# Kernel tuning notes

Hardware: AMD Instinct MI355X
Metric: run time of the kernel (lower is better)

## Reference

```python
import jax, jax.numpy as jnp
import numpy as np

N_NODES = 100000
N_EDGES = 640000
IN_FEATS = 128
OUT_FEATS = 128


def setup_inputs() -> dict:
    key = jax.random.key(0)
    k1, k2, k3 = jax.random.split(key, 3)
    feat = jax.random.normal(k1, (N_NODES, IN_FEATS), dtype=jnp.float32)
    edge_src = jax.random.randint(k2, (N_EDGES,), 0, N_NODES, dtype=jnp.int64)
    edge_dst = jax.random.randint(k3, (N_EDGES,), 0, N_NODES, dtype=jnp.int64)
    # init.constant_(weight, 1) / init.constant_(bias, 1) in the original module
    weight = jnp.ones((OUT_FEATS, IN_FEATS), dtype=jnp.float32)
    bias = jnp.ones((OUT_FEATS,), dtype=jnp.float32)
    return {"feat": feat, "edge_src": edge_src, "edge_dst": edge_dst,
            "weight": weight, "bias": bias}


def reference(feat, edge_src, edge_dst, weight, bias):
    # copy_u: message on each edge is the source node's feature  [E, F_in]
    msgs = feat[edge_src]
    # sum reduce messages into destination nodes                 [N_V, F_in]
    h = jax.ops.segment_sum(msgs, edge_dst, num_segments=N_NODES)
    # linear: h @ W^T + b                                        [N_V, F_out]
    return h @ weight.T + bias
```

## Files before the change

kernel.cpp:

```cpp
#include <hip/hip_runtime.h>

#define F 128
#define STRIDE 32

typedef __bf16 bf8 __attribute__((ext_vector_type(8)));
typedef __bf16 bf4 __attribute__((ext_vector_type(4)));
typedef float f4 __attribute__((ext_vector_type(4)));
typedef unsigned short us8 __attribute__((ext_vector_type(8)));

__global__ void zero_int(int* __restrict__ p, int n) {
  int i = blockIdx.x * blockDim.x + threadIdx.x;
  if (i < n) p[i] = 0;
}

__global__ void zero_f4(float4* __restrict__ p, int n4) {
  int i = blockIdx.x * blockDim.x + threadIdx.x;
  if (i < n4) p[i] = make_float4(0.f, 0.f, 0.f, 0.f);
}

__global__ __launch_bounds__(256, 4) void transform_build(
    const float* __restrict__ feat, const float* __restrict__ W,
    __bf16* __restrict__ tf, const int* __restrict__ esrc,
    const int* __restrict__ edst, int* __restrict__ cnt,
    int* __restrict__ bucket, int n_rows, int nN, int nE) {
  __shared__ bf8 wlds[2048];
  const int tid = threadIdx.x;
  const int lane = tid & 63;
  const int wid = tid >> 6;
  const int lr = lane & 15;
  const int hi = lane >> 4;
  const int lk = hi * 8;

  const int e0 = blockIdx.x * 512 + tid;
  const int e1 = e0 + 256;
  int d0 = -1, d1 = -1, s0 = 0, s1 = 0;
  if (e0 < nE) { d0 = edst[e0]; s0 = esrc[e0]; }
  if (e1 < nE) { d1 = edst[e1]; s1 = esrc[e1]; }

  const int r0 = blockIdx.x * 64 + wid * 16;
  int arow = r0 + lr;
  if (arow >= n_rows) arow = n_rows - 1;
  if (arow < 0) arow = 0;
  const float* hr = feat + (size_t)arow * F;
  float4 u[8];
#pragma unroll
  for (int kk = 0; kk < 4; ++kk) {
    u[kk * 2]     = *(const float4*)(hr + kk * 32 + lk);
    u[kk * 2 + 1] = *(const float4*)(hr + kk * 32 + lk + 4);
  }

  int p0 = (d0 >= 0) ? atomicAdd(&cnt[d0], 1) : STRIDE;
  int p1 = (d1 >= 0) ? atomicAdd(&cnt[d1], 1) : STRIDE;

#pragma unroll
  for (int i = 0; i < 8; ++i) {
    int fid = tid + i * 256;
    int fl = fid & 63;
    int kkt = fid >> 6;
    int kk = kkt & 3;
    int t = kkt >> 2;
    const float* wr = W + (size_t)(t * 16 + (fl & 15)) * F + kk * 32 + (fl >> 4) * 8;
    float4 w0 = *(const float4*)wr;
    float4 w1 = *(const float4*)(wr + 4);
    bf8 b;
    b[0] = (__bf16)w0.x; b[1] = (__bf16)w0.y;
    b[2] = (__bf16)w0.z; b[3] = (__bf16)w0.w;
    b[4] = (__bf16)w1.x; b[5] = (__bf16)w1.y;
    b[6] = (__bf16)w1.z; b[7] = (__bf16)w1.w;
    wlds[fid] = b;
  }
  __syncthreads();

  if (p0 < STRIDE) bucket[(size_t)p0 * nN + d0] = s0;
  if (p1 < STRIDE) bucket[(size_t)p1 * nN + d1] = s1;

  if (r0 >= n_rows) return;

  bf8 af[4];
#pragma unroll
  for (int kk = 0; kk < 4; ++kk) {
    bf8 a;
    a[0] = (__bf16)u[kk * 2].x;     a[1] = (__bf16)u[kk * 2].y;
    a[2] = (__bf16)u[kk * 2].z;     a[3] = (__bf16)u[kk * 2].w;
    a[4] = (__bf16)u[kk * 2 + 1].x; a[5] = (__bf16)u[kk * 2 + 1].y;
    a[6] = (__bf16)u[kk * 2 + 1].z; a[7] = (__bf16)u[kk * 2 + 1].w;
    af[kk] = a;
  }

  f4 acc[8];
#pragma unroll
  for (int t = 0; t < 8; ++t) acc[t] = (f4){0.f, 0.f, 0.f, 0.f};
#pragma unroll
  for (int kk = 0; kk < 4; ++kk)
#pragma unroll
    for (int t = 0; t < 8; ++t)
      acc[t] = __builtin_amdgcn_mfma_f32_16x16x32_bf16(
          wlds[(t * 4 + kk) * 64 + lane], af[kk], acc[t], 0, 0, 0);

  const int r = r0 + lr;
  if (r < n_rows) {
    __bf16* dst = tf + (size_t)r * F + hi * 4;
#pragma unroll
    for (int t = 0; t < 8; ++t) {
      bf4 p;
      p[0] = (__bf16)acc[t][0];
      p[1] = (__bf16)acc[t][1];
      p[2] = (__bf16)acc[t][2];
      p[3] = (__bf16)acc[t][3];
      *(bf4*)(dst + t * 16) = p;
    }
  }
}

__device__ inline void addrow(float* a, us8 v) {
#pragma unroll
  for (int j = 0; j < 8; ++j) a[j] += __uint_as_float((unsigned)v[j] << 16);
}

__global__ __launch_bounds__(256) void aggregate_bf16(
    const __bf16* __restrict__ tf, const int* __restrict__ cnt,
    const int* __restrict__ bucket, const float* __restrict__ bias,
    float* __restrict__ out, int nN) {
  long long gid = (long long)blockIdx.x * 256 + threadIdx.x;
  int node = (int)(gid >> 4);
  int c = (int)(gid & 15);
  if (node >= nN) return;
  int n = cnt[node];
  if (n > STRIDE) n = STRIDE;
  const us8* t8 = (const us8*)tf;
  float4 b0 = ((const float4*)bias)[c * 2];
  float4 b1 = ((const float4*)bias)[c * 2 + 1];
  float a[8] = {b0.x, b0.y, b0.z, b0.w, b1.x, b1.y, b1.z, b1.w};
  int k = 0;
  for (; k + 3 < n; k += 4) {
    int s0 = bucket[(size_t)k * nN + node];
    int s1 = bucket[(size_t)(k + 1) * nN + node];
    int s2 = bucket[(size_t)(k + 2) * nN + node];
    int s3 = bucket[(size_t)(k + 3) * nN + node];
    us8 v0 = t8[(size_t)s0 * 16 + c];
    us8 v1 = t8[(size_t)s1 * 16 + c];
    us8 v2 = t8[(size_t)s2 * 16 + c];
    us8 v3 = t8[(size_t)s3 * 16 + c];
    addrow(a, v0);
    addrow(a, v1);
    addrow(a, v2);
    addrow(a, v3);
  }
  if (k + 1 < n) {
    int s0 = bucket[(size_t)k * nN + node];
    int s1 = bucket[(size_t)(k + 1) * nN + node];
    us8 v0 = t8[(size_t)s0 * 16 + c];
    us8 v1 = t8[(size_t)s1 * 16 + c];
    addrow(a, v0);
    addrow(a, v1);
    k += 2;
  }
  if (k < n) {
    int s0 = bucket[(size_t)k * nN + node];
    us8 v0 = t8[(size_t)s0 * 16 + c];
    addrow(a, v0);
  }
  float4* o = (float4*)out + (size_t)node * 32 + c * 2;
  o[0] = make_float4(a[0], a[1], a[2], a[3]);
  o[1] = make_float4(a[4], a[5], a[6], a[7]);
}

__global__ __launch_bounds__(256) void scatter_add(
    const float* __restrict__ feat, const int* __restrict__ src,
    const int* __restrict__ dst, float* __restrict__ h, int n_edges) {
  long long gid = (long long)blockIdx.x * 256 + threadIdx.x;
  int e = (int)(gid >> 5);
  if (e >= n_edges) return;
  int c = (int)(gid & 31);
  int s = src[e];
  int d = dst[e];
  float4 v = reinterpret_cast<const float4*>(feat + (long long)s * F)[c];
  float* hp = h + (long long)d * F + c * 4;
  __hip_atomic_fetch_add(hp + 0, v.x, __ATOMIC_RELAXED, __HIP_MEMORY_SCOPE_AGENT);
  __hip_atomic_fetch_add(hp + 1, v.y, __ATOMIC_RELAXED, __HIP_MEMORY_SCOPE_AGENT);
  __hip_atomic_fetch_add(hp + 2, v.z, __ATOMIC_RELAXED, __HIP_MEMORY_SCOPE_AGENT);
  __hip_atomic_fetch_add(hp + 3, v.w, __ATOMIC_RELAXED, __HIP_MEMORY_SCOPE_AGENT);
}

__global__ __launch_bounds__(256, 2) void gemm_bias_inplace(
    float* __restrict__ hout, const float* __restrict__ W,
    const float* __restrict__ bias, int n_rows, int n_groups) {
  const int lane = threadIdx.x & 63;
  const int wid = threadIdx.x >> 6;
  const int lr = lane & 15;
  const int lk = (lane >> 4) * 8;
  bf8 wf[8][4];
#pragma unroll
  for (int t = 0; t < 8; ++t) {
    const float* wr = W + (size_t)(t * 16 + lr) * F;
#pragma unroll
    for (int kk = 0; kk < 4; ++kk) {
      float4 u0 = *(const float4*)(wr + kk * 32 + lk);
      float4 u1 = *(const float4*)(wr + kk * 32 + lk + 4);
      bf8 b;
      b[0] = (__bf16)u0.x; b[1] = (__bf16)u0.y;
      b[2] = (__bf16)u0.z; b[3] = (__bf16)u0.w;
      b[4] = (__bf16)u1.x; b[5] = (__bf16)u1.y;
      b[6] = (__bf16)u1.z; b[7] = (__bf16)u1.w;
      wf[t][kk] = b;
    }
  }
  float bj[8];
#pragma unroll
  for (int t = 0; t < 8; ++t) bj[t] = bias[t * 16 + lr];
  for (int g = blockIdx.x; g < n_groups; g += gridDim.x) {
    const int r0 = g * 64 + wid * 16;
    if (r0 >= n_rows) continue;
    int arow = r0 + lr;
    if (arow >= n_rows) arow = n_rows - 1;
    const float* hr = hout + (size_t)arow * F;
    bf8 af[4];
#pragma unroll
    for (int kk = 0; kk < 4; ++kk) {
      float4 u0 = *(const float4*)(hr + kk * 32 + lk);
      float4 u1 = *(const float4*)(hr + kk * 32 + lk + 4);
      bf8 a;
      a[0] = (__bf16)u0.x; a[1] = (__bf16)u0.y;
      a[2] = (__bf16)u0.z; a[3] = (__bf16)u0.w;
      a[4] = (__bf16)u1.x; a[5] = (__bf16)u1.y;
      a[6] = (__bf16)u1.z; a[7] = (__bf16)u1.w;
      af[kk] = a;
    }
    f4 acc[8];
#pragma unroll
    for (int t = 0; t < 8; ++t) acc[t] = (f4){bj[t], bj[t], bj[t], bj[t]};
#pragma unroll
    for (int kk = 0; kk < 4; ++kk)
#pragma unroll
      for (int t = 0; t < 8; ++t)
        acc[t] = __builtin_amdgcn_mfma_f32_16x16x32_bf16(af[kk], wf[t][kk],
                                                         acc[t], 0, 0, 0);
    const int rbase = r0 + (lane >> 4) * 4;
#pragma unroll
    for (int t = 0; t < 8; ++t)
#pragma unroll
      for (int i = 0; i < 4; ++i) {
        int r = rbase + i;
        if (r < n_rows) hout[(size_t)r * F + t * 16 + lr] = acc[t][i];
      }
  }
}

static inline size_t align_up(size_t x, size_t a) { return (x + a - 1) & ~(a - 1); }

extern "C" void kernel_launch(void* const* d_in, const int* in_sizes, int n_in,
                              void* d_out, int out_size, void* d_ws, size_t ws_size,
                              hipStream_t stream) {
  const float* feat = (const float*)d_in[0];
  const int* esrc   = (const int*)d_in[1];
  const int* edst   = (const int*)d_in[2];
  const float* W    = (const float*)d_in[3];
  const float* bias = (const float*)d_in[4];
  float* out = (float*)d_out;

  const int nE = in_sizes[1];
  const int nN = out_size / F;

  size_t off_cnt  = 0;
  size_t off_bkt  = align_up(off_cnt + (size_t)nN * 4, 256);
  size_t off_tf   = align_up(off_bkt + (size_t)nN * STRIDE * 4, 256);
  size_t need     = off_tf + (size_t)nN * F * 2;
  const int n_groups = (nN + 63) / 64;

  if (ws_size >= need) {
    char* w = (char*)d_ws;
    int* cnt    = (int*)(w + off_cnt);
    int* bucket = (int*)(w + off_bkt);
    __bf16* tf  = (__bf16*)(w + off_tf);

    zero_int<<<(nN + 255) / 256, 256, 0, stream>>>(cnt, nN);

    const int e_blocks = (nE + 511) / 512;
    const int tb_blocks = n_groups > e_blocks ? n_groups : e_blocks;
    transform_build<<<tb_blocks, 256, 0, stream>>>(feat, W, tf, esrc, edst,
                                                   cnt, bucket, nN, nN, nE);

    long long thr = (long long)nN * 16;
    aggregate_bf16<<<(int)((thr + 255) / 256), 256, 0, stream>>>(
        tf, cnt, bucket, bias, out, nN);
  } else {
    int n4 = out_size / 4;
    zero_f4<<<(n4 + 255) / 256, 256, 0, stream>>>((float4*)out, n4);
    long long total = (long long)nE * 32;
    scatter_add<<<(int)((total + 255) / 256), 256, 0, stream>>>(feat, esrc,
                                                                edst, out, nE);
    gemm_bias_inplace<<<640, 256, 0, stream>>>(out, W, bias, nN, n_groups);
  }
}
```

Baseline: 91.30 us.

## Partition edge bucketing by destination range per block group for atomic locality

Replaces the one-edge-per-thread bucketing with a scheme where blocks are split into eight groups, each owning one destination-node range. Each block scans a contiguous chunk of edges with vectorized int4 loads and does atomics and bucket writes only for destinations in its range. The grid now equals the number of 64-row transform groups. The aim is better L2 locality for the cnt atomics and bucket scatter, possibly relevant on MI355X's partitioned cache. In exchange every edge is read eight times and the edge pass now runs after the MFMA transform in the same block.

```diff
diff --git a/kernel.cpp b/kernel.cpp
--- a/kernel.cpp
+++ b/kernel.cpp
@@ -22,7 +22,7 @@
     const float* __restrict__ feat, const float* __restrict__ W,
     __bf16* __restrict__ tf, const int* __restrict__ esrc,
     const int* __restrict__ edst, int* __restrict__ cnt,
-    int* __restrict__ bucket, int n_rows, int nN, int nE) {
+    int* __restrict__ bucket, int n_rows, int nN, int nE, int rng) {
   __shared__ bf8 wlds[2048];
   const int tid = threadIdx.x;
   const int lane = tid & 63;
@@ -31,16 +31,9 @@
   const int hi = lane >> 4;
   const int lk = hi * 8;
 
-  const int e0 = blockIdx.x * 512 + tid;
-  const int e1 = e0 + 256;
-  int d0 = -1, d1 = -1, s0 = 0, s1 = 0;
-  if (e0 < nE) { d0 = edst[e0]; s0 = esrc[e0]; }
-  if (e1 < nE) { d1 = edst[e1]; s1 = esrc[e1]; }
-
   const int r0 = blockIdx.x * 64 + wid * 16;
   int arow = r0 + lr;
   if (arow >= n_rows) arow = n_rows - 1;
-  if (arow < 0) arow = 0;
   const float* hr = feat + (size_t)arow * F;
   float4 u[8];
 #pragma unroll
@@ -48,9 +41,6 @@
     u[kk * 2]     = *(const float4*)(hr + kk * 32 + lk);
     u[kk * 2 + 1] = *(const float4*)(hr + kk * 32 + lk + 4);
   }
-
-  int p0 = (d0 >= 0) ? atomicAdd(&cnt[d0], 1) : STRIDE;
-  int p1 = (d1 >= 0) ? atomicAdd(&cnt[d1], 1) : STRIDE;
 
 #pragma unroll
   for (int i = 0; i < 8; ++i) {
@@ -71,43 +61,72 @@
   }
   __syncthreads();
 
-  if (p0 < STRIDE) bucket[(size_t)p0 * nN + d0] = s0;
-  if (p1 < STRIDE) bucket[(size_t)p1 * nN + d1] = s1;
-
-  if (r0 >= n_rows) return;
-
-  bf8 af[4];
-#pragma unroll
-  for (int kk = 0; kk < 4; ++kk) {
-    bf8 a;
-    a[0] = (__bf16)u[kk * 2].x;     a[1] = (__bf16)u[kk * 2].y;
-    a[2] = (__bf16)u[kk * 2].z;     a[3] = (__bf16)u[kk * 2].w;
-    a[4] = (__bf16)u[kk * 2 + 1].x; a[5] = (__bf16)u[kk * 2 + 1].y;
-    a[6] = (__bf16)u[kk * 2 + 1].z; a[7] = (__bf16)u[kk * 2 + 1].w;
-    af[kk] = a;
-  }
-
-  f4 acc[8];
-#pragma unroll
-  for (int t = 0; t < 8; ++t) acc[t] = (f4){0.f, 0.f, 0.f, 0.f};
-#pragma unroll
-  for (int kk = 0; kk < 4; ++kk)
-#pragma unroll
-    for (int t = 0; t < 8; ++t)
-      acc[t] = __builtin_amdgcn_mfma_f32_16x16x32_bf16(
-          wlds[(t * 4 + kk) * 64 + lane], af[kk], acc[t], 0, 0, 0);
-
-  const int r = r0 + lr;
-  if (r < n_rows) {
-    __bf16* dst = tf + (size_t)r * F + hi * 4;
-#pragma unroll
-    for (int t = 0; t < 8; ++t) {
-      bf4 p;
-      p[0] = (__bf16)acc[t][0];
-      p[1] = (__bf16)acc[t][1];
-      p[2] = (__bf16)acc[t][2];
-      p[3] = (__bf16)acc[t][3];
-      *(bf4*)(dst + t * 16) = p;
+  if (r0 < n_rows) {
+    bf8 af[4];
+#pragma unroll
+    for (int kk = 0; kk < 4; ++kk) {
+      bf8 a;
+      a[0] = (__bf16)u[kk * 2].x;     a[1] = (__bf16)u[kk * 2].y;
+      a[2] = (__bf16)u[kk * 2].z;     a[3] = (__bf16)u[kk * 2].w;
+      a[4] = (__bf16)u[kk * 2 + 1].x; a[5] = (__bf16)u[kk * 2 + 1].y;
+      a[6] = (__bf16)u[kk * 2 + 1].z; a[7] = (__bf16)u[kk * 2 + 1].w;
+      af[kk] = a;
+    }
+    f4 acc[8];
+#pragma unroll
+    for (int t = 0; t < 8; ++t) acc[t] = (f4){0.f, 0.f, 0.f, 0.f};
+#pragma unroll
+    for (int kk = 0; kk < 4; ++kk)
+#pragma unroll
+      for (int t = 0; t < 8; ++t)
+        acc[t] = __builtin_amdgcn_mfma_f32_16x16x32_bf16(
+            wlds[(t * 4 + kk) * 64 + lane], af[kk], acc[t], 0, 0, 0);
+    const int r = r0 + lr;
+    if (r < n_rows) {
+      __bf16* dst = tf + (size_t)r * F + hi * 4;
+#pragma unroll
+      for (int t = 0; t < 8; ++t) {
+        bf4 p;
+        p[0] = (__bf16)acc[t][0];
+        p[1] = (__bf16)acc[t][1];
+        p[2] = (__bf16)acc[t][2];
+        p[3] = (__bf16)acc[t][3];
+        *(bf4*)(dst + t * 16) = p;
+      }
+    }
+  }
+
+  const int x = blockIdx.x & 7;
+  const int q = blockIdx.x >> 3;
+  const int nc = (int)(((int)gridDim.x - 1 - x) >> 3) + 1;
+  const int lo = x * rng;
+  const int hi2 = min(nN, lo + rng);
+  long long chunk = ((long long)nE + nc - 1) / nc;
+  chunk = (chunk + 3) & ~3LL;
+  const int ebeg = (int)((long long)q * chunk);
+  const int eend = (int)min((long long)nE, (long long)ebeg + chunk);
+  for (int e = ebeg + tid * 4; e < eend; e += 1024) {
+    int d[4], s[4];
+    if (e + 3 < eend) {
+      int4 dv = *(const int4*)(edst + e);
+      int4 sv = *(const int4*)(esrc + e);
+      d[0] = dv.x; d[1] = dv.y; d[2] = dv.z; d[3] = dv.w;
+      s[0] = sv.x; s[1] = sv.y; s[2] = sv.z; s[3] = sv.w;
+    } else {
+      int m = eend - e;
+#pragma unroll
+      for (int j = 0; j < 4; ++j) {
+        d[j] = (j < m) ? edst[e + j] : -1;
+        s[j] = (j < m) ? esrc[e + j] : 0;
+      }
+    }
+#pragma unroll
+    for (int j = 0; j < 4; ++j) {
+      int dd = d[j];
+      if (dd >= lo && dd < hi2) {
+        int p = atomicAdd(&cnt[dd], 1);
+        if (p < STRIDE) bucket[(size_t)p * nN + dd] = s[j];
+      }
     }
   }
 }
@@ -275,10 +294,9 @@
 
     zero_int<<<(nN + 255) / 256, 256, 0, stream>>>(cnt, nN);
 
-    const int e_blocks = (nE + 511) / 512;
-    const int tb_blocks = n_groups > e_blocks ? n_groups : e_blocks;
-    transform_build<<<tb_blocks, 256, 0, stream>>>(feat, W, tf, esrc, edst,
-                                                   cnt, bucket, nN, nN, nE);
+    const int rng = (nN + 7) / 8;
+    transform_build<<<n_groups, 256, 0, stream>>>(feat, W, tf, esrc, edst,
+                                                  cnt, bucket, nN, nN, nE, rng);
 
     long long thr = (long long)nN * 16;
     aggregate_bf16<<<(int)((thr + 255) / 256), 256, 0, stream>>>(
```

New measurement: 93.30 us. 1.02x slower.

## Store edge buckets node-major and split edge and transform blocks

Applied to the files above, without the earlier changes.

The bucket array moves from slot-major (slot*nN+node) to node-major (node*STRIDE+slot), so aggregation can read eight neighbor indices with two int4 loads instead of strided scalar loads. The fused kernel now gives edge-bucketing and feature-transform work to separate block ranges instead of having every block do both, so blocks no longer mix atomics with MFMA work. The aggregation loop is restructured to issue up to eight gathers before accumulating. Bucket writes become scattered per node, and the int4 reads may pass the valid count, though those lanes are masked.

```diff
diff --git a/kernel.cpp b/kernel.cpp
--- a/kernel.cpp
+++ b/kernel.cpp
@@ -18,29 +18,37 @@
   if (i < n4) p[i] = make_float4(0.f, 0.f, 0.f, 0.f);
 }
 
-__global__ __launch_bounds__(256, 4) void transform_build(
+__global__ __launch_bounds__(256, 4) void fused_main(
     const float* __restrict__ feat, const float* __restrict__ W,
     __bf16* __restrict__ tf, const int* __restrict__ esrc,
     const int* __restrict__ edst, int* __restrict__ cnt,
-    int* __restrict__ bucket, int n_rows, int nN, int nE) {
+    int* __restrict__ bucket, int n_rows, int nE, int e_blocks) {
   __shared__ bf8 wlds[2048];
   const int tid = threadIdx.x;
+
+  if ((int)blockIdx.x < e_blocks) {
+    const int e0 = blockIdx.x * 512 + tid;
+    const int e1 = e0 + 256;
+    int d0 = -1, d1 = -1, s0 = 0, s1 = 0;
+    if (e0 < nE) { d0 = edst[e0]; s0 = esrc[e0]; }
+    if (e1 < nE) { d1 = edst[e1]; s1 = esrc[e1]; }
+    int p0 = (d0 >= 0) ? atomicAdd(&cnt[d0], 1) : STRIDE;
+    int p1 = (d1 >= 0) ? atomicAdd(&cnt[d1], 1) : STRIDE;
+    if (p0 < STRIDE) bucket[(size_t)d0 * STRIDE + p0] = s0;
+    if (p1 < STRIDE) bucket[(size_t)d1 * STRIDE + p1] = s1;
+    return;
+  }
+
+  const int g = blockIdx.x - e_blocks;
   const int lane = tid & 63;
   const int wid = tid >> 6;
   const int lr = lane & 15;
   const int hi = lane >> 4;
   const int lk = hi * 8;
 
-  const int e0 = blockIdx.x * 512 + tid;
-  const int e1 = e0 + 256;
-  int d0 = -1, d1 = -1, s0 = 0, s1 = 0;
-  if (e0 < nE) { d0 = edst[e0]; s0 = esrc[e0]; }
-  if (e1 < nE) { d1 = edst[e1]; s1 = esrc[e1]; }
-
-  const int r0 = blockIdx.x * 64 + wid * 16;
+  const int r0 = g * 64 + wid * 16;
   int arow = r0 + lr;
   if (arow >= n_rows) arow = n_rows - 1;
-  if (arow < 0) arow = 0;
   const float* hr = feat + (size_t)arow * F;
   float4 u[8];
 #pragma unroll
@@ -48,9 +56,6 @@
     u[kk * 2]     = *(const float4*)(hr + kk * 32 + lk);
     u[kk * 2 + 1] = *(const float4*)(hr + kk * 32 + lk + 4);
   }
-
-  int p0 = (d0 >= 0) ? atomicAdd(&cnt[d0], 1) : STRIDE;
-  int p1 = (d1 >= 0) ? atomicAdd(&cnt[d1], 1) : STRIDE;
 
 #pragma unroll
   for (int i = 0; i < 8; ++i) {
@@ -71,9 +76,6 @@
   }
   __syncthreads();
 
-  if (p0 < STRIDE) bucket[(size_t)p0 * nN + d0] = s0;
-  if (p1 < STRIDE) bucket[(size_t)p1 * nN + d1] = s1;
-
   if (r0 >= n_rows) return;
 
   bf8 af[4];
@@ -86,7 +88,6 @@
     a[6] = (__bf16)u[kk * 2 + 1].z; a[7] = (__bf16)u[kk * 2 + 1].w;
     af[kk] = a;
   }
-
   f4 acc[8];
 #pragma unroll
   for (int t = 0; t < 8; ++t) acc[t] = (f4){0.f, 0.f, 0.f, 0.f};
@@ -128,37 +129,22 @@
   int n = cnt[node];
   if (n > STRIDE) n = STRIDE;
   const us8* t8 = (const us8*)tf;
+  const int4* bk = (const int4*)(bucket + (size_t)node * STRIDE);
   float4 b0 = ((const float4*)bias)[c * 2];
   float4 b1 = ((const float4*)bias)[c * 2 + 1];
   float a[8] = {b0.x, b0.y, b0.z, b0.w, b1.x, b1.y, b1.z, b1.w};
-  int k = 0;
-  for (; k + 3 < n; k += 4) {
-    int s0 = bucket[(size_t)k * nN + node];
-    int s1 = bucket[(size_t)(k + 1) * nN + node];
-    int s2 = bucket[(size_t)(k + 2) * nN + node];
-    int s3 = bucket[(size_t)(k + 3) * nN + node];
-    us8 v0 = t8[(size_t)s0 * 16 + c];
-    us8 v1 = t8[(size_t)s1 * 16 + c];
-    us8 v2 = t8[(size_t)s2 * 16 + c];
-    us8 v3 = t8[(size_t)s3 * 16 + c];
-    addrow(a, v0);
-    addrow(a, v1);
-    addrow(a, v2);
-    addrow(a, v3);
-  }
-  if (k + 1 < n) {
-    int s0 = bucket[(size_t)k * nN + node];
-    int s1 = bucket[(size_t)(k + 1) * nN + node];
-    us8 v0 = t8[(size_t)s0 * 16 + c];
-    us8 v1 = t8[(size_t)s1 * 16 + c];
-    addrow(a, v0);
-    addrow(a, v1);
-    k += 2;
-  }
-  if (k < n) {
-    int s0 = bucket[(size_t)k * nN + node];
-    us8 v0 = t8[(size_t)s0 * 16 + c];
-    addrow(a, v0);
+  for (int k = 0; k < n; k += 8) {
+    const int m = n - k;
+    int4 q0 = bk[k >> 2];
+    int4 q1 = bk[(k >> 2) + 1];
+    int s[8] = {q0.x, q0.y, q0.z, q0.w, q1.x, q1.y, q1.z, q1.w};
+    us8 v[8];
+#pragma unroll
+    for (int j = 0; j < 8; ++j)
+      if (j < m) v[j] = t8[(size_t)s[j] * 16 + c];
+#pragma unroll
+    for (int j = 0; j < 8; ++j)
+      if (j < m) addrow(a, v[j]);
   }
   float4* o = (float4*)out + (size_t)node * 32 + c * 2;
   o[0] = make_float4(a[0], a[1], a[2], a[3]);
@@ -276,9 +262,8 @@
     zero_int<<<(nN + 255) / 256, 256, 0, stream>>>(cnt, nN);
 
     const int e_blocks = (nE + 511) / 512;
-    const int tb_blocks = n_groups > e_blocks ? n_groups : e_blocks;
-    transform_build<<<tb_blocks, 256, 0, stream>>>(feat, W, tf, esrc, edst,
-                                                   cnt, bucket, nN, nN, nE);
+    fused_main<<<e_blocks + n_groups, 256, 0, stream>>>(
+        feat, W, tf, esrc, edst, cnt, bucket, nN, nE, e_blocks);
 
     long long thr = (long long)nN * 16;
     aggregate_bf16<<<(int)((thr + 255) / 256), 256, 0, stream>>>(
```

Result: slower. 104.2 us (+14.1%).
